# Kernel tuning notes

Hardware: AMD Instinct MI355X
Metric: run time of the kernel (lower is better)

## Reference

```python
import jax, jax.numpy as jnp
import numpy as np


def _gather_neighbours(h, idx):
    # h: (B, N, H); idx: (B, N, K) int -> (B, N, K, H)
    B, N, H = h.shape
    K = idx.shape[-1]
    flat = idx.reshape(B, N * K)  # (B, N*K)
    rep = jnp.take_along_axis(h, flat[..., None], axis=1)  # (B, N*K, H)
    return rep.reshape(B, N, K, H)


def _masked_agg(h, idx, mask):
    # gather neighbor hidden states then masked sum over neighbors -> (B, N, H)
    rep = _gather_neighbours(h, idx)
    return jnp.einsum('bnkh,bnk->bnh', rep, mask)


def setup_inputs() -> dict:
    key = jax.random.key(0)
    ks = jax.random.split(key, 12)
    B, N, H, K = 8, 2000, 128, 32
    s = 1.0 / np.sqrt(H)
    return {
        'node_hidden': jax.random.normal(ks[0], (B, N, H), jnp.float32),
        'cell': jax.random.normal(ks[1], (B, N, H), jnp.float32),
        'w_in': jax.random.normal(ks[2], (4, H, H), jnp.float32) * s,
        'w_out': jax.random.normal(ks[3], (4, H, H), jnp.float32) * s,
        'u_in': jax.random.normal(ks[4], (4, H, H), jnp.float32) * s,
        'u_out': jax.random.normal(ks[5], (4, H, H), jnp.float32) * s,
        'b': jax.random.normal(ks[6], (4, H), jnp.float32) * 0.1,
        'in_node_mask': jax.random.uniform(ks[7], (B, N, K), jnp.float32),
        'out_node_mask': jax.random.uniform(ks[8], (B, N, K), jnp.float32),
        'in_node_index': jax.random.randint(ks[9], (B, N, K), 0, N, jnp.int32),
        'out_node_index': jax.random.randint(ks[10], (B, N, K), 0, N, jnp.int32),
        'layer_num': 2,
    }


def reference(node_hidden, cell, w_in, w_out, u_in, u_out, b,
              in_node_mask, out_node_mask, in_node_index, out_node_index,
              layer_num):
    h, c = node_hidden, cell
    for _ in range(layer_num):
        in_agg = _masked_agg(h, in_node_index, in_node_mask)    # (B,N,H)
        out_agg = _masked_agg(h, out_node_index, out_node_mask)  # (B,N,H)
        # gate pre-activations, gate order: i, o, f, cell
        pre = (jnp.einsum('bnh,ghd->gbnd', in_agg, w_in)
               + jnp.einsum('bnh,ghd->gbnd', out_agg, w_out)
               + jnp.einsum('bnh,ghd->gbnd', h, u_in)
               + jnp.einsum('bnh,ghd->gbnd', h, u_out)
               + b[:, None, None, :])
        i_g = jax.nn.sigmoid(pre[0])
        o_g = jax.nn.sigmoid(pre[1])
        f_g = jax.nn.sigmoid(pre[2])
        g = jnp.tanh(pre[3])
        c = f_g * c + i_g * g
        h = o_g * jnp.tanh(c)
    return h
```

## Files before the change

kernel.cpp:

```cpp
#include <hip/hip_runtime.h>
#include <math.h>

#define B_ 8
#define N_ 2000
#define H_ 128
#define K_ 32
#define M_ (B_*N_)
#define KTOT 384
#define NC 512
#define NTILES 32
#define NCHUNK 12
#define AGG_BLOCKS (M_ / 8)
#define PREP_BLOCKS (NTILES * NCHUNK)
#define GEMM_BLOCKS 1024

typedef __attribute__((ext_vector_type(8))) short s8_t;
typedef __attribute__((ext_vector_type(4))) float f4_t;

__device__ __forceinline__ unsigned short f2bf(float x) {
    union { float f; unsigned u; } v; v.f = x;
    unsigned r = v.u + 0x7fff + ((v.u >> 16) & 1);
    return (unsigned short)(r >> 16);
}
__device__ __forceinline__ float bf2f(unsigned short b) {
    union { unsigned u; float f; } v; v.u = (unsigned)b << 16; return v.f;
}
__device__ __forceinline__ float sigm_(float x) { return 1.f / (1.f + __expf(-x)); }
__device__ __forceinline__ float tanh_(float x) { return 2.f / (1.f + __expf(-2.f * x)) - 1.f; }

__device__ __forceinline__ float pickv(f4_t A, int m) {
    float ab = (m & 1) ? A.y : A.x;
    float cd = (m & 1) ? A.w : A.z;
    return (m & 2) ? cd : ab;
}
__device__ __forceinline__ float pick4(float u0, float u1, float u2, float u3, int m) {
    float ab = (m & 1) ? u1 : u0;
    float cd = (m & 1) ? u3 : u2;
    return (m & 2) ? cd : ab;
}

__device__ __forceinline__ void split4(const float* f, ushort4& hi, ushort4& lo) {
    unsigned short h0 = f2bf(f[0]), h1 = f2bf(f[1]), h2 = f2bf(f[2]), h3 = f2bf(f[3]);
    hi = make_ushort4(h0, h1, h2, h3);
    lo = make_ushort4(f2bf(f[0] - bf2f(h0)), f2bf(f[1] - bf2f(h1)),
                      f2bf(f[2] - bf2f(h2)), f2bf(f[3] - bf2f(h3)));
}

__device__ __forceinline__ void gload_lds(const unsigned short* g, short* l) {
    __builtin_amdgcn_global_load_lds(
        (const __attribute__((address_space(1))) unsigned*)g,
        (__attribute__((address_space(3))) unsigned*)l, 16, 0, 0);
}

__device__ __forceinline__ void prep_elem(int pb, int t,
                                          const float* __restrict__ w_in,
                                          const float* __restrict__ w_out,
                                          const float* __restrict__ u_in,
                                          const float* __restrict__ u_out,
                                          unsigned short* __restrict__ wp_hi,
                                          unsigned short* __restrict__ wp_lo) {
    int ntile = pb / NCHUNK, chunk = pb % NCHUNK;
    int lane = t >> 3, e = t & 7;
    int col = ntile * 16 + (lane & 15);
    int k = chunk * 32 + (lane >> 4) * 8 + e;
    int d = col >> 2, g = col & 3;
    float v;
    if (k < 128) {
        v = w_in[(g * 128 + k) * 128 + d];
    } else if (k < 256) {
        v = w_out[(g * 128 + (k - 128)) * 128 + d];
    } else {
        int kk = k - 256;
        v = u_in[(g * 128 + kk) * 128 + d] + u_out[(g * 128 + kk) * 128 + d];
    }
    unsigned short hs = f2bf(v);
    wp_hi[(size_t)pb * 512 + t] = hs;
    wp_lo[(size_t)pb * 512 + t] = f2bf(v - bf2f(hs));
}

__device__ __forceinline__ void agg_body(int a, int tid,
                                         const float* __restrict__ h,
                                         const int* __restrict__ in_idx,
                                         const float* __restrict__ in_mask,
                                         const int* __restrict__ out_idx,
                                         const float* __restrict__ out_mask,
                                         unsigned short* __restrict__ A_hi,
                                         unsigned short* __restrict__ A_lo,
                                         int (*s_idx)[64], float (*s_msk)[64]) {
    int r = tid >> 5;
    int p = tid & 31;
    int row = a * 8 + r;
    int b = row / N_;
    const float* hb = h + (size_t)b * N_ * H_;

    for (int e = tid; e < 512; e += 256) {
        int r2 = e >> 6, q = e & 63;
        int ridx = a * 8 + r2;
        if (q < 32) {
            s_idx[r2][q] = in_idx[ridx * K_ + q];
            s_msk[r2][q] = in_mask[ridx * K_ + q];
        } else {
            s_idx[r2][q] = out_idx[ridx * K_ + (q - 32)];
            s_msk[r2][q] = out_mask[ridx * K_ + (q - 32)];
        }
    }
    __syncthreads();

    int d0 = p * 4;
    float ai[4] = {0.f, 0.f, 0.f, 0.f};
    float ao[4] = {0.f, 0.f, 0.f, 0.f};
    #pragma unroll 16
    for (int k = 0; k < K_; ++k) {
        int   i1 = s_idx[r][k];
        float m1 = s_msk[r][k];
        int   i2 = s_idx[r][32 + k];
        float m2 = s_msk[r][32 + k];
        float4 v1 = *(const float4*)(hb + (size_t)i1 * H_ + d0);
        float4 v2 = *(const float4*)(hb + (size_t)i2 * H_ + d0);
        ai[0] += m1 * v1.x; ai[1] += m1 * v1.y; ai[2] += m1 * v1.z; ai[3] += m1 * v1.w;
        ao[0] += m2 * v2.x; ao[1] += m2 * v2.y; ao[2] += m2 * v2.z; ao[3] += m2 * v2.w;
    }
    float4 hv4 = *(const float4*)(h + (size_t)row * H_ + d0);
    float hh[4] = {hv4.x, hv4.y, hv4.z, hv4.w};

    int mtile = row >> 4;
    int kg = (p >> 1) & 3;
    int e0 = (p & 1) * 4;
    int lane = (row & 15) + 16 * kg;
    size_t bi = ((size_t)(mtile * NCHUNK +     (p >> 3)) * 64 + lane) * 8 + e0;
    size_t bo = ((size_t)(mtile * NCHUNK + 4 + (p >> 3)) * 64 + lane) * 8 + e0;
    size_t bh = ((size_t)(mtile * NCHUNK + 8 + (p >> 3)) * 64 + lane) * 8 + e0;

    ushort4 hi, lo;
    split4(ai, hi, lo); *(ushort4*)(A_hi + bi) = hi; *(ushort4*)(A_lo + bi) = lo;
    split4(ao, hi, lo); *(ushort4*)(A_hi + bo) = hi; *(ushort4*)(A_lo + bo) = lo;
    split4(hh, hi, lo); *(ushort4*)(A_hi + bh) = hi; *(ushort4*)(A_lo + bh) = lo;
}

__global__ __launch_bounds__(256)
void agg0_prep_kernel(const float* __restrict__ h,
                      const int* __restrict__ in_idx,
                      const float* __restrict__ in_mask,
                      const int* __restrict__ out_idx,
                      const float* __restrict__ out_mask,
                      unsigned short* __restrict__ A_hi,
                      unsigned short* __restrict__ A_lo,
                      const float* __restrict__ w_in,
                      const float* __restrict__ w_out,
                      const float* __restrict__ u_in,
                      const float* __restrict__ u_out,
                      unsigned short* __restrict__ wp_hi,
                      unsigned short* __restrict__ wp_lo) {
    __shared__ int   s_idx[8][64];
    __shared__ float s_msk[8][64];
    int tid = threadIdx.x;
    if (blockIdx.x < AGG_BLOCKS) {
        int bid = (blockIdx.x & 7) * 250 + (blockIdx.x >> 3);
        agg_body(bid, tid, h, in_idx, in_mask, out_idx, out_mask,
                 A_hi, A_lo, s_idx, s_msk);
    } else {
        int pb = blockIdx.x - AGG_BLOCKS;
        prep_elem(pb, tid,       w_in, w_out, u_in, u_out, wp_hi, wp_lo);
        prep_elem(pb, tid + 256, w_in, w_out, u_in, u_out, wp_hi, wp_lo);
    }
}

__global__ __launch_bounds__(256)
void agg_kernel(const float* __restrict__ h,
                const int* __restrict__ in_idx,
                const float* __restrict__ in_mask,
                const int* __restrict__ out_idx,
                const float* __restrict__ out_mask,
                unsigned short* __restrict__ A_hi,
                unsigned short* __restrict__ A_lo) {
    __shared__ int   s_idx[8][64];
    __shared__ float s_msk[8][64];
    int bid = (blockIdx.x & 7) * 250 + (blockIdx.x >> 3);
    agg_body(bid, threadIdx.x, h, in_idx, in_mask, out_idx, out_mask,
             A_hi, A_lo, s_idx, s_msk);
}

__global__ __launch_bounds__(256)
void gemm_gates(const unsigned short* __restrict__ A_hi,
                const unsigned short* __restrict__ A_lo,
                const unsigned short* __restrict__ wp_hi,
                const unsigned short* __restrict__ wp_lo,
                const float* __restrict__ bias,
                const float* __restrict__ c_src,
                float* __restrict__ c_dst,
                float* __restrict__ h_dst,
                int write_c) {
    __shared__ short sL[24 * 512];
    int l = blockIdx.x;
    int x = l & 7;
    int s_slot = l >> 3;
    int mt_lo  = x ? ((2000 * x + 63) >> 7) : 0;
    int mt_nxt = (2000 * (x + 1) + 63) >> 7;
    int cnt = (mt_nxt - mt_lo) * 8;
    if (s_slot >= cnt) return;
    int mt = mt_lo + (s_slot >> 3);
    int jt = s_slot & 7;

    int tid  = threadIdx.x;
    int lane = tid & 63;
    int w    = tid >> 6;
    int wm   = w & 1;
    int wn   = w >> 1;
    int mtile0 = mt * 8;
    int ntile0 = jt * 4;

    const unsigned short* gp[6];
    short* lp[6];
    #pragma unroll
    for (int i = 0; i < 6; ++i) {
        int s = i * 4 + w;
        const unsigned short* src;
        if (s < 8)       src = A_hi  + ((size_t)((mtile0 + s)      * NCHUNK) * 64 + lane) * 8;
        else if (s < 16) src = A_lo  + ((size_t)((mtile0 + s - 8)  * NCHUNK) * 64 + lane) * 8;
        else if (s < 20) src = wp_hi + ((size_t)((ntile0 + s - 16) * NCHUNK) * 64 + lane) * 8;
        else             src = wp_lo + ((size_t)((ntile0 + s - 20) * NCHUNK) * 64 + lane) * 8;
        gp[i] = src;
        lp[i] = &sL[s * 512];
    }

    f4_t zero = {0.f, 0.f, 0.f, 0.f};
    f4_t acc[4][2];
    #pragma unroll
    for (int i = 0; i < 4; ++i)
        #pragma unroll
        for (int j = 0; j < 2; ++j) acc[i][j] = zero;

    #pragma unroll 1
    for (int c = 0; c < NCHUNK; ++c) {
        if (c > 0) __syncthreads();
        #pragma unroll
        for (int i = 0; i < 6; ++i) {
            gload_lds(gp[i], lp[i]);
            gp[i] += 512;
        }
        __syncthreads();

        s8_t a_hi[4], a_lo[4], b_hi[2], b_lo[2];
        #pragma unroll
        for (int i = 0; i < 4; ++i) {
            a_hi[i] = *(const s8_t*)&sL[(wm * 4 + i) * 512 + lane * 8];
            a_lo[i] = *(const s8_t*)&sL[(8 + wm * 4 + i) * 512 + lane * 8];
        }
        #pragma unroll
        for (int j = 0; j < 2; ++j) {
            b_hi[j] = *(const s8_t*)&sL[(16 + wn * 2 + j) * 512 + lane * 8];
            b_lo[j] = *(const s8_t*)&sL[(20 + wn * 2 + j) * 512 + lane * 8];
        }
        #pragma unroll
        for (int i = 0; i < 4; ++i)
            #pragma unroll
            for (int j = 0; j < 2; ++j) {
                acc[i][j] = __builtin_amdgcn_mfma_f32_16x16x32_bf16(a_hi[i], b_hi[j], acc[i][j], 0, 0, 0);
                acc[i][j] = __builtin_amdgcn_mfma_f32_16x16x32_bf16(a_hi[i], b_lo[j], acc[i][j], 0, 0, 0);
                acc[i][j] = __builtin_amdgcn_mfma_f32_16x16x32_bf16(a_lo[i], b_hi[j], acc[i][j], 0, 0, 0);
            }
    }

    int g    = lane & 3;
    int qrow = lane >> 4;
    int dl   = (lane >> 2) & 3;
    #pragma unroll
    for (int j = 0; j < 2; ++j) {
        int ncol_base = jt * 64 + wn * 32 + j * 16;
        int d = (ncol_base >> 2) + dl;
        float b0 = bias[0 * 128 + d];
        float b1 = bias[1 * 128 + d];
        float b2 = bias[2 * 128 + d];
        float b3 = bias[3 * 128 + d];
        #pragma unroll
        for (int i = 0; i < 4; ++i) {
            f4_t A = acc[i][j];
            float s0 = pickv(A, g);
            float s1 = pickv(A, g ^ 1);
            float s2 = pickv(A, g ^ 2);
            float s3 = pickv(A, g ^ 3);
            float u0 = s0;
            float u1 = __shfl_xor(s1, 1);
            float u2 = __shfl_xor(s2, 2);
            float u3 = __shfl_xor(s3, 3);
            float p0 = pick4(u0, u1, u2, u3, g) + b0;
            float p1 = pick4(u0, u1, u2, u3, g ^ 1) + b1;
            float p2 = pick4(u0, u1, u2, u3, g ^ 2) + b2;
            float p3 = pick4(u0, u1, u2, u3, g ^ 3) + b3;
            float ig = sigm_(p0);
            float og = sigm_(p1);
            float fg = sigm_(p2);
            float cg = tanh_(p3);
            int row = mt * 128 + wm * 64 + i * 16 + qrow * 4 + g;
            size_t off = (size_t)row * H_ + d;
            float c_old = c_src[off];
            float c_new = fg * c_old + ig * cg;
            if (write_c) c_dst[off] = c_new;
            h_dst[off] = og * tanh_(c_new);
        }
    }
}

extern "C" void kernel_launch(void* const* d_in, const int* in_sizes, int n_in,
                              void* d_out, int out_size, void* d_ws, size_t ws_size,
                              hipStream_t stream) {
    const float* node_hidden = (const float*)d_in[0];
    const float* cell        = (const float*)d_in[1];
    const float* w_in        = (const float*)d_in[2];
    const float* w_out       = (const float*)d_in[3];
    const float* u_in        = (const float*)d_in[4];
    const float* u_out       = (const float*)d_in[5];
    const float* bias        = (const float*)d_in[6];
    const float* in_mask     = (const float*)d_in[7];
    const float* out_mask    = (const float*)d_in[8];
    const int*   in_idx      = (const int*)d_in[9];
    const int*   out_idx     = (const int*)d_in[10];
    float* out = (float*)d_out;

    char* p = (char*)d_ws;
    unsigned short* wp_hi = (unsigned short*)p; p += (size_t)NTILES * NCHUNK * 512 * 2;
    unsigned short* wp_lo = (unsigned short*)p; p += (size_t)NTILES * NCHUNK * 512 * 2;
    unsigned short* A_hi  = (unsigned short*)p; p += (size_t)(M_/16) * NCHUNK * 512 * 2;
    unsigned short* A_lo  = (unsigned short*)p; p += (size_t)(M_/16) * NCHUNK * 512 * 2;
    float* h_buf = (float*)p;                   p += (size_t)M_ * H_ * 4;

    agg0_prep_kernel<<<AGG_BLOCKS + PREP_BLOCKS, 256, 0, stream>>>(
        node_hidden, in_idx, in_mask, out_idx, out_mask, A_hi, A_lo,
        w_in, w_out, u_in, u_out, wp_hi, wp_lo);
    gemm_gates<<<GEMM_BLOCKS, 256, 0, stream>>>(
        A_hi, A_lo, wp_hi, wp_lo, bias, cell, out, h_buf, 1);

    agg_kernel<<<AGG_BLOCKS, 256, 0, stream>>>(h_buf, in_idx, in_mask,
                                               out_idx, out_mask, A_hi, A_lo);
    gemm_gates<<<GEMM_BLOCKS, 256, 0, stream>>>(
        A_hi, A_lo, wp_hi, wp_lo, bias, out, out, out, 0);
}
```

Before: 178.0 us.

## Load GEMM fragments directly into registers with double-buffered prefetch, drop LDS staging

The gate GEMM no longer stages A and weight fragments through shared memory with global_load_lds and two barriers per chunk. Each wave now loads its own pre-packed fragments straight from global memory into registers, using a two-deep register double buffer so the next chunk's loads overlap the current chunk's MFMAs. This removes the LDS round trip and block-wide synchronisation. In exchange, weight and A fragments shared across waves are fetched redundantly from global/L2, and register pressure rises.

```diff
diff --git a/kernel.cpp b/kernel.cpp
--- a/kernel.cpp
+++ b/kernel.cpp
@@ -44,12 +44,6 @@
     hi = make_ushort4(h0, h1, h2, h3);
     lo = make_ushort4(f2bf(f[0] - bf2f(h0)), f2bf(f[1] - bf2f(h1)),
                       f2bf(f[2] - bf2f(h2)), f2bf(f[3] - bf2f(h3)));
-}
-
-__device__ __forceinline__ void gload_lds(const unsigned short* g, short* l) {
-    __builtin_amdgcn_global_load_lds(
-        (const __attribute__((address_space(1))) unsigned*)g,
-        (__attribute__((address_space(3))) unsigned*)l, 16, 0, 0);
 }
 
 __device__ __forceinline__ void prep_elem(int pb, int t,
@@ -180,6 +174,39 @@
              A_hi, A_lo, s_idx, s_msk);
 }
 
+__device__ __forceinline__ void load_chunk(
+        const unsigned short* const (&pa_hi)[4],
+        const unsigned short* const (&pa_lo)[4],
+        const unsigned short* const (&pb_hi)[2],
+        const unsigned short* const (&pb_lo)[2],
+        int c,
+        s8_t (&ah)[4], s8_t (&al)[4], s8_t (&bh)[2], s8_t (&bl)[2]) {
+    #pragma unroll
+    for (int i = 0; i < 4; ++i) {
+        ah[i] = *(const s8_t*)(pa_hi[i] + (size_t)c * 512);
+        al[i] = *(const s8_t*)(pa_lo[i] + (size_t)c * 512);
+    }
+    #pragma unroll
+    for (int j = 0; j < 2; ++j) {
+        bh[j] = *(const s8_t*)(pb_hi[j] + (size_t)c * 512);
+        bl[j] = *(const s8_t*)(pb_lo[j] + (size_t)c * 512);
+    }
+}
+
+__device__ __forceinline__ void mfma_chunk(
+        const s8_t (&ah)[4], const s8_t (&al)[4],
+        const s8_t (&bh)[2], const s8_t (&bl)[2],
+        f4_t (&acc)[4][2]) {
+    #pragma unroll
+    for (int i = 0; i < 4; ++i)
+        #pragma unroll
+        for (int j = 0; j < 2; ++j) {
+            acc[i][j] = __builtin_amdgcn_mfma_f32_16x16x32_bf16(ah[i], bh[j], acc[i][j], 0, 0, 0);
+            acc[i][j] = __builtin_amdgcn_mfma_f32_16x16x32_bf16(ah[i], bl[j], acc[i][j], 0, 0, 0);
+            acc[i][j] = __builtin_amdgcn_mfma_f32_16x16x32_bf16(al[i], bh[j], acc[i][j], 0, 0, 0);
+        }
+}
+
 __global__ __launch_bounds__(256)
 void gemm_gates(const unsigned short* __restrict__ A_hi,
                 const unsigned short* __restrict__ A_lo,
@@ -190,7 +217,6 @@
                 float* __restrict__ c_dst,
                 float* __restrict__ h_dst,
                 int write_c) {
-    __shared__ short sL[24 * 512];
     int l = blockIdx.x;
     int x = l & 7;
     int s_slot = l >> 3;
@@ -209,18 +235,21 @@
     int mtile0 = mt * 8;
     int ntile0 = jt * 4;
 
-    const unsigned short* gp[6];
-    short* lp[6];
-    #pragma unroll
-    for (int i = 0; i < 6; ++i) {
-        int s = i * 4 + w;
-        const unsigned short* src;
-        if (s < 8)       src = A_hi  + ((size_t)((mtile0 + s)      * NCHUNK) * 64 + lane) * 8;
-        else if (s < 16) src = A_lo  + ((size_t)((mtile0 + s - 8)  * NCHUNK) * 64 + lane) * 8;
-        else if (s < 20) src = wp_hi + ((size_t)((ntile0 + s - 16) * NCHUNK) * 64 + lane) * 8;
-        else             src = wp_lo + ((size_t)((ntile0 + s - 20) * NCHUNK) * 64 + lane) * 8;
-        gp[i] = src;
-        lp[i] = &sL[s * 512];
+    const unsigned short* pa_hi[4];
+    const unsigned short* pa_lo[4];
+    const unsigned short* pb_hi[2];
+    const unsigned short* pb_lo[2];
+    #pragma unroll
+    for (int i = 0; i < 4; ++i) {
+        size_t off = (size_t)(mtile0 + wm * 4 + i) * (NCHUNK * 512) + lane * 8;
+        pa_hi[i] = A_hi + off;
+        pa_lo[i] = A_lo + off;
+    }
+    #pragma unroll
+    for (int j = 0; j < 2; ++j) {
+        size_t off = (size_t)(ntile0 + wn * 2 + j) * (NCHUNK * 512) + lane * 8;
+        pb_hi[j] = wp_hi + off;
+        pb_lo[j] = wp_lo + off;
     }
 
     f4_t zero = {0.f, 0.f, 0.f, 0.f};
@@ -230,36 +259,19 @@
         #pragma unroll
         for (int j = 0; j < 2; ++j) acc[i][j] = zero;
 
+    s8_t ah0[4], al0[4], bh0[2], bl0[2];
+    s8_t ah1[4], al1[4], bh1[2], bl1[2];
+    load_chunk(pa_hi, pa_lo, pb_hi, pb_lo, 0, ah0, al0, bh0, bl0);
     #pragma unroll 1
-    for (int c = 0; c < NCHUNK; ++c) {
-        if (c > 0) __syncthreads();
-        #pragma unroll
-        for (int i = 0; i < 6; ++i) {
-            gload_lds(gp[i], lp[i]);
-            gp[i] += 512;
-        }
-        __syncthreads();
-
-        s8_t a_hi[4], a_lo[4], b_hi[2], b_lo[2];
-        #pragma unroll
-        for (int i = 0; i < 4; ++i) {
-            a_hi[i] = *(const s8_t*)&sL[(wm * 4 + i) * 512 + lane * 8];
-            a_lo[i] = *(const s8_t*)&sL[(8 + wm * 4 + i) * 512 + lane * 8];
-        }
-        #pragma unroll
-        for (int j = 0; j < 2; ++j) {
-            b_hi[j] = *(const s8_t*)&sL[(16 + wn * 2 + j) * 512 + lane * 8];
-            b_lo[j] = *(const s8_t*)&sL[(20 + wn * 2 + j) * 512 + lane * 8];
-        }
-        #pragma unroll
-        for (int i = 0; i < 4; ++i)
-            #pragma unroll
-            for (int j = 0; j < 2; ++j) {
-                acc[i][j] = __builtin_amdgcn_mfma_f32_16x16x32_bf16(a_hi[i], b_hi[j], acc[i][j], 0, 0, 0);
-                acc[i][j] = __builtin_amdgcn_mfma_f32_16x16x32_bf16(a_hi[i], b_lo[j], acc[i][j], 0, 0, 0);
-                acc[i][j] = __builtin_amdgcn_mfma_f32_16x16x32_bf16(a_lo[i], b_hi[j], acc[i][j], 0, 0, 0);
-            }
-    }
+    for (int c = 0; c < NCHUNK - 2; c += 2) {
+        load_chunk(pa_hi, pa_lo, pb_hi, pb_lo, c + 1, ah1, al1, bh1, bl1);
+        mfma_chunk(ah0, al0, bh0, bl0, acc);
+        load_chunk(pa_hi, pa_lo, pb_hi, pb_lo, c + 2, ah0, al0, bh0, bl0);
+        mfma_chunk(ah1, al1, bh1, bl1, acc);
+    }
+    load_chunk(pa_hi, pa_lo, pb_hi, pb_lo, NCHUNK - 1, ah1, al1, bh1, bl1);
+    mfma_chunk(ah0, al0, bh0, bl0, acc);
+    mfma_chunk(ah1, al1, bh1, bl1, acc);
 
     int g    = lane & 3;
     int qrow = lane >> 4;
```

After: 191.4 us. +7.5%, slower.

## Double-buffer LDS chunks in gate GEMM to overlap global loads with MFMA

Applied to the files above, without the earlier changes.

The gate GEMM now uses two LDS buffers and prefetches the next K-chunk with global-to-LDS loads while the current chunk's fragments are read and multiplied. Synchronisation uses explicit vmcnt/lgkmcnt waits and raw barriers in place of __syncthreads. Launch bounds now request 3 blocks per CU. The aim is to hide global load latency behind MFMA work, at the cost of doubled LDS per block (48KB), which may limit occupancy.

```diff
diff --git a/kernel.cpp b/kernel.cpp
--- a/kernel.cpp
+++ b/kernel.cpp
@@ -13,6 +13,7 @@
 #define AGG_BLOCKS (M_ / 8)
 #define PREP_BLOCKS (NTILES * NCHUNK)
 #define GEMM_BLOCKS 1024
+#define CH_SH (24 * 512)
 
 typedef __attribute__((ext_vector_type(8))) short s8_t;
 typedef __attribute__((ext_vector_type(4))) float f4_t;
@@ -180,7 +181,36 @@
              A_hi, A_lo, s_idx, s_msk);
 }
 
-__global__ __launch_bounds__(256)
+__device__ __forceinline__ void frag_load(const short* sb, int wm, int wn, int lane,
+                                          s8_t (&ah)[4], s8_t (&al)[4],
+                                          s8_t (&bh)[2], s8_t (&bl)[2]) {
+    #pragma unroll
+    for (int i = 0; i < 4; ++i) {
+        ah[i] = *(const s8_t*)&sb[(wm * 4 + i) * 512 + lane * 8];
+        al[i] = *(const s8_t*)&sb[(8 + wm * 4 + i) * 512 + lane * 8];
+    }
+    #pragma unroll
+    for (int j = 0; j < 2; ++j) {
+        bh[j] = *(const s8_t*)&sb[(16 + wn * 2 + j) * 512 + lane * 8];
+        bl[j] = *(const s8_t*)&sb[(20 + wn * 2 + j) * 512 + lane * 8];
+    }
+}
+
+__device__ __forceinline__ void mfma_chunk(
+        const s8_t (&ah)[4], const s8_t (&al)[4],
+        const s8_t (&bh)[2], const s8_t (&bl)[2],
+        f4_t (&acc)[4][2]) {
+    #pragma unroll
+    for (int i = 0; i < 4; ++i)
+        #pragma unroll
+        for (int j = 0; j < 2; ++j) {
+            acc[i][j] = __builtin_amdgcn_mfma_f32_16x16x32_bf16(ah[i], bh[j], acc[i][j], 0, 0, 0);
+            acc[i][j] = __builtin_amdgcn_mfma_f32_16x16x32_bf16(ah[i], bl[j], acc[i][j], 0, 0, 0);
+            acc[i][j] = __builtin_amdgcn_mfma_f32_16x16x32_bf16(al[i], bh[j], acc[i][j], 0, 0, 0);
+        }
+}
+
+__global__ __launch_bounds__(256, 3)
 void gemm_gates(const unsigned short* __restrict__ A_hi,
                 const unsigned short* __restrict__ A_lo,
                 const unsigned short* __restrict__ wp_hi,
@@ -190,7 +220,7 @@
                 float* __restrict__ c_dst,
                 float* __restrict__ h_dst,
                 int write_c) {
-    __shared__ short sL[24 * 512];
+    __shared__ short sL[2 * CH_SH];
     int l = blockIdx.x;
     int x = l & 7;
     int s_slot = l >> 3;
@@ -210,7 +240,8 @@
     int ntile0 = jt * 4;
 
     const unsigned short* gp[6];
-    short* lp[6];
+    short* lpA[6];
+    short* lpB[6];
     #pragma unroll
     for (int i = 0; i < 6; ++i) {
         int s = i * 4 + w;
@@ -220,7 +251,8 @@
         else if (s < 20) src = wp_hi + ((size_t)((ntile0 + s - 16) * NCHUNK) * 64 + lane) * 8;
         else             src = wp_lo + ((size_t)((ntile0 + s - 20) * NCHUNK) * 64 + lane) * 8;
         gp[i] = src;
-        lp[i] = &sL[s * 512];
+        lpA[i] = &sL[s * 512];
+        lpB[i] = &sL[CH_SH + s * 512];
     }
 
     f4_t zero = {0.f, 0.f, 0.f, 0.f};
@@ -230,35 +262,40 @@
         #pragma unroll
         for (int j = 0; j < 2; ++j) acc[i][j] = zero;
 
+    s8_t ah[4], al[4], bh[2], bl[2];
+
+    #pragma unroll
+    for (int i = 0; i < 6; ++i) { gload_lds(gp[i], lpA[i]); gp[i] += 512; }
+
     #pragma unroll 1
-    for (int c = 0; c < NCHUNK; ++c) {
-        if (c > 0) __syncthreads();
-        #pragma unroll
-        for (int i = 0; i < 6; ++i) {
-            gload_lds(gp[i], lp[i]);
-            gp[i] += 512;
-        }
-        __syncthreads();
-
-        s8_t a_hi[4], a_lo[4], b_hi[2], b_lo[2];
-        #pragma unroll
-        for (int i = 0; i < 4; ++i) {
-            a_hi[i] = *(const s8_t*)&sL[(wm * 4 + i) * 512 + lane * 8];
-            a_lo[i] = *(const s8_t*)&sL[(8 + wm * 4 + i) * 512 + lane * 8];
-        }
-        #pragma unroll
-        for (int j = 0; j < 2; ++j) {
-            b_hi[j] = *(const s8_t*)&sL[(16 + wn * 2 + j) * 512 + lane * 8];
-            b_lo[j] = *(const s8_t*)&sL[(20 + wn * 2 + j) * 512 + lane * 8];
-        }
-        #pragma unroll
-        for (int i = 0; i < 4; ++i)
+    for (int c = 0; c < NCHUNK; c += 2) {
+        if (c + 1 < NCHUNK) {
             #pragma unroll
-            for (int j = 0; j < 2; ++j) {
-                acc[i][j] = __builtin_amdgcn_mfma_f32_16x16x32_bf16(a_hi[i], b_hi[j], acc[i][j], 0, 0, 0);
-                acc[i][j] = __builtin_amdgcn_mfma_f32_16x16x32_bf16(a_hi[i], b_lo[j], acc[i][j], 0, 0, 0);
-                acc[i][j] = __builtin_amdgcn_mfma_f32_16x16x32_bf16(a_lo[i], b_hi[j], acc[i][j], 0, 0, 0);
-            }
+            for (int i = 0; i < 6; ++i) { gload_lds(gp[i], lpB[i]); gp[i] += 512; }
+            asm volatile("s_waitcnt vmcnt(6)" ::: "memory");
+        } else {
+            asm volatile("s_waitcnt vmcnt(0)" ::: "memory");
+        }
+        asm volatile("s_barrier" ::: "memory");
+        frag_load(sL, wm, wn, lane, ah, al, bh, bl);
+        asm volatile("s_waitcnt lgkmcnt(0)" ::: "memory");
+        __builtin_amdgcn_sched_barrier(0);
+        asm volatile("s_barrier" ::: "memory");
+        mfma_chunk(ah, al, bh, bl, acc);
+
+        if (c + 2 < NCHUNK) {
+            #pragma unroll
+            for (int i = 0; i < 6; ++i) { gload_lds(gp[i], lpA[i]); gp[i] += 512; }
+            asm volatile("s_waitcnt vmcnt(6)" ::: "memory");
+        } else {
+            asm volatile("s_waitcnt vmcnt(0)" ::: "memory");
+        }
+        asm volatile("s_barrier" ::: "memory");
+        frag_load(sL + CH_SH, wm, wn, lane, ah, al, bh, bl);
+        asm volatile("s_waitcnt lgkmcnt(0)" ::: "memory");
+        __builtin_amdgcn_sched_barrier(0);
+        asm volatile("s_barrier" ::: "memory");
+        mfma_chunk(ah, al, bh, bl, acc);
     }
 
     int g    = lane & 3;
```

Result: slower. 185.3 us (+4.1%).
